# Optimization experiments

Measured on AMD Instinct MI355X. Metric: run time of the kernel, lower is better.

## Reference

```python
import jax, jax.numpy as jnp
import numpy as np

N_BRANCH, N_LAYER = 4, 3
B, T, D_IN = 4, 1024, 32
D_MODEL, D_INNER, D_STATE, D_CONV, DT_RANK = 128, 256, 16, 4, 8
EMBED = 64
MAX_NORM = 10.0  # safe_expmap0 tangent-norm clip
EPS = 1e-7


def setup_inputs() -> dict:
    key = jax.random.key(0)
    ks = jax.random.split(key, 12)
    def nrm(k, shp, s=0.02):
        return s * jax.random.normal(k, shp, dtype=jnp.float32)
    A_init = jnp.log(jnp.arange(1, D_STATE + 1, dtype=jnp.float32))
    return {
        "trend": jax.random.normal(ks[0], (B, T, D_IN), jnp.float32),
        "seasonal_coarse": jax.random.normal(ks[1], (B, T, D_IN), jnp.float32),
        "seasonal_fine": jax.random.normal(ks[2], (B, T, D_IN), jnp.float32),
        "residual": jax.random.normal(ks[3], (B, T, D_IN), jnp.float32),
        "W_ip": nrm(ks[4], (N_BRANCH, D_IN, D_MODEL)),
        "b_ip": jnp.zeros((N_BRANCH, D_MODEL), jnp.float32),
        "W_in": nrm(ks[5], (N_BRANCH, N_LAYER, D_MODEL, 2 * D_INNER)),
        "conv_w": nrm(ks[6], (N_BRANCH, N_LAYER, D_INNER, D_CONV), 0.1),
        "conv_b": jnp.zeros((N_BRANCH, N_LAYER, D_INNER), jnp.float32),
        "W_x": nrm(ks[7], (N_BRANCH, N_LAYER, D_INNER, DT_RANK + 2 * D_STATE)),
        "W_dt": nrm(ks[8], (N_BRANCH, N_LAYER, DT_RANK, D_INNER), 0.1),
        "b_dt": jnp.full((N_BRANCH, N_LAYER, D_INNER), -4.6, jnp.float32),  # softplus ~ 0.01
        "A_log": jnp.broadcast_to(A_init, (N_BRANCH, N_LAYER, D_INNER, D_STATE)),
        "D_param": jnp.ones((N_BRANCH, N_LAYER, D_INNER), jnp.float32),
        "W_out": nrm(ks[9], (N_BRANCH, N_LAYER, D_INNER, D_MODEL)),
        "W_op": nrm(ks[10], (N_BRANCH, D_MODEL, EMBED)),
        "b_op": jnp.zeros((N_BRANCH, EMBED), jnp.float32),
        "eff_scale": jnp.asarray(0.1, jnp.float32),
    }


def _mamba_layer(x, Win, cw, cb, Wx, Wdt, bdt, Alog, Dp, Wout):
    # x: [B, T, d_model]
    Tlen = x.shape[1]
    xz = x @ Win                                   # [B,T,2*di]
    xp, z = jnp.split(xz, 2, axis=-1)
    # causal depthwise conv1d, kernel D_CONV
    xpad = jnp.pad(xp, ((0, 0), (D_CONV - 1, 0), (0, 0)))
    xc = sum(xpad[:, k:k + Tlen, :] * cw[:, k] for k in range(D_CONV))
    xc = jax.nn.silu(xc + cb)                      # [B,T,di]
    dbl = xc @ Wx                                  # [B,T,r+2s]
    dt = jax.nn.softplus(dbl[..., :DT_RANK] @ Wdt + bdt)   # [B,T,di]
    Bm = dbl[..., DT_RANK:DT_RANK + D_STATE]       # [B,T,s]
    Cm = dbl[..., DT_RANK + D_STATE:]              # [B,T,s]
    A = -jnp.exp(Alog)                             # [di,s]
    dA = jnp.exp(dt[..., None] * A)                # [B,T,di,s]
    dBx = (dt * xc)[..., None] * Bm[:, :, None, :] # [B,T,di,s]

    def step(h, inp):
        dA_t, dBx_t, C_t = inp
        h = dA_t * h + dBx_t
        return h, jnp.einsum('bds,bs->bd', h, C_t)

    h0 = jnp.zeros((x.shape[0], D_INNER, D_STATE), x.dtype)
    _, ys = jax.lax.scan(step, h0, (jnp.swapaxes(dA, 0, 1),
                                     jnp.swapaxes(dBx, 0, 1),
                                     jnp.swapaxes(Cm, 0, 1)))
    y = jnp.swapaxes(ys, 0, 1) + Dp * xc
    return (y * jax.nn.silu(z)) @ Wout


def _embed(x, Wip, bip, Wins, cws, cbs, Wxs, Wdts, bdts, Alogs, Dps, Wouts, Wop, bop):
    h = x @ Wip + bip
    for l in range(N_LAYER):
        h = _mamba_layer(h, Wins[l], cws[l], cbs[l], Wxs[l], Wdts[l], bdts[l],
                         Alogs[l], Dps[l], Wouts[l])
    return h.mean(axis=1) @ Wop + bop              # [B, EMBED]


def _expmap0(v):
    # safe expmap0 on Lorentz (k=1): clip tangent norm at MAX_NORM
    n = jnp.linalg.norm(v, axis=-1, keepdims=True)
    nc = jnp.clip(n, EPS, MAX_NORM)
    v = v * (nc / jnp.maximum(n, EPS))
    return jnp.concatenate([jnp.cosh(nc), jnp.sinh(nc) / nc * v], axis=-1)


def _projx(x):
    sp = x[..., 1:]
    t = jnp.sqrt(1.0 + jnp.sum(sp * sp, axis=-1, keepdims=True))
    return jnp.concatenate([t, sp], axis=-1)


def _logmap0(x):
    sp = x[..., 1:]
    t = jnp.maximum(x[..., :1], 1.0 + EPS)
    d = jnp.arccosh(t)
    spn = jnp.maximum(jnp.linalg.norm(sp, axis=-1, keepdims=True), EPS)
    return d * sp / spn


def _forward(trend, seasonal_coarse, seasonal_fine, residual,
             W_ip, b_ip, W_in, conv_w, conv_b, W_x, W_dt, b_dt,
             A_log, D_param, W_out, W_op, b_op, eff_scale):
    xs = [trend, seasonal_coarse, seasonal_fine, residual]
    z_t = [
        _embed(xs[b], W_ip[b], b_ip[b], W_in[b], conv_w[b], conv_b[b], W_x[b],
               W_dt[b], b_dt[b], A_log[b], D_param[b], W_out[b], W_op[b], b_op[b])
        for b in range(N_BRANCH)
    ]
    es = jnp.tanh(eff_scale)
    z_h = [_projx(_expmap0(z * es)) for z in z_t]
    us = [_logmap0(zh) for zh in z_h]
    combined_tangent = us[0] + us[1] + us[2] + us[3]
    combined_h = _projx(_expmap0(combined_tangent * es))
    return (*z_t, *z_h, combined_tangent, combined_h)


def reference(trend, seasonal_coarse, seasonal_fine, residual,
              W_ip, b_ip, W_in, conv_w, conv_b, W_x, W_dt, b_dt,
              A_log, D_param, W_out, W_op, b_op, eff_scale):
    return _forward(trend, seasonal_coarse, seasonal_fine, residual,
                    W_ip, b_ip, W_in, conv_w, conv_b, W_x, W_dt, b_dt,
                    A_log, D_param, W_out, W_op, b_op, eff_scale)
```

## Files before the change

kernel.cpp:

```cpp
#include <hip/hip_runtime.h>
#include <math.h>

#define NBR 4
#define NLAY 3
#define Bk 4
#define Tk 1024
#define DIN 32
#define DMODEL 128
#define DINNER 256
#define DSTATE 16
#define DTRANK 8
#define EMBEDk 64
#define BT (Bk*Tk)
#define EPSF 1e-7f
#define MAXNF 10.0f
#define LCH 64
#define NCH (Tk/LCH)
#define UF 8
#define NWB 320

typedef __bf16 bf16x8 __attribute__((ext_vector_type(8)));
typedef float  f32x4  __attribute__((ext_vector_type(4)));
typedef unsigned short u16x8 __attribute__((ext_vector_type(8)));
typedef unsigned short u16x4 __attribute__((ext_vector_type(4)));

__device__ __forceinline__ float siluf(float x){ return x / (1.f + __expf(-x)); }
__device__ __forceinline__ float softplusf(float x){ return (x > 20.f) ? x : log1pf(__expf(x)); }
__device__ __forceinline__ unsigned short f2b(float x){
    union { float f; unsigned u; } v; v.f = x;
    unsigned r = v.u + 0x7FFF + ((v.u >> 16) & 1);
    return (unsigned short)(r >> 16);
}
__device__ __forceinline__ float b2f(unsigned short u){
    union { unsigned u; float f; } v; v.u = ((unsigned)u) << 16; return v.f;
}

__device__ __forceinline__ void gll16(const void* g, void* l){
    __builtin_amdgcn_global_load_lds(
        (const __attribute__((address_space(1))) unsigned int*)g,
        (__attribute__((address_space(3))) unsigned int*)l,
        16, 0, 0);
}

__device__ __forceinline__ void dA_pow(float q, float* dA){
    dA[0] = q;             dA[1] = q * q;
    dA[2] = dA[1] * dA[0]; dA[3] = dA[1] * dA[1];
    dA[4] = dA[3] * dA[0]; dA[5] = dA[3] * dA[1];
    dA[6] = dA[3] * dA[2]; dA[7] = dA[3] * dA[3];
    #pragma unroll
    for (int s = 8; s < 16; ++s) dA[s] = dA[s - 8] * dA[7];
}
__device__ __forceinline__ void dA_exp(float dtv, const float* Aa, float* dA){
    #pragma unroll
    for (int s = 0; s < 16; ++s) dA[s] = __expf(dtv * Aa[s]);
}

template<int MODE>
__global__ __launch_bounds__(256) void bgemm_k(
    const unsigned short* __restrict__ Ab, long aBr, int K,
    const unsigned short* __restrict__ Bt, long bBr,
    float* __restrict__ C0, long c0Br,
    float* __restrict__ C1, long c1Br,
    unsigned short* __restrict__ Cb, long cbBr,
    const float* __restrict__ bias, long biasBr)
{
    const int br = blockIdx.z;
    Ab += (long)br * aBr;
    Bt += (long)br * bBr;
    if (MODE == 3) C0 += (long)br * c0Br;
    if (MODE == 0 || MODE == 3) C1 += (long)br * c1Br;
    if (MODE == 0) Cb += (long)br * cbBr;
    if (MODE == 3) bias += (long)br * biasBr;
    const int m0 = blockIdx.x * 64, n0 = blockIdx.y * 64;
    __shared__ __align__(16) unsigned short As[8 * 64 * 8];
    __shared__ __align__(16) unsigned short Bs[8 * 64 * 8];
    const int tid = threadIdx.x;
    const int lane = tid & 63, w = tid >> 6;
    const int wm = w >> 1, wn = w & 1;
    const int quad = lane >> 4, l15 = lane & 15;
    f32x4 acc00 = {0,0,0,0}, acc01 = {0,0,0,0}, acc10 = {0,0,0,0}, acc11 = {0,0,0,0};
    for (int kc = 0; kc < K; kc += 64) {
        #pragma unroll
        for (int it = 0; it < 2; ++it) {
            const int kch = w + it * 4;
            gll16(Ab + (long)(m0 + lane) * K + kc + kch * 8, &As[(kch * 64) * 8]);
            gll16(Bt + (long)(n0 + lane) * K + kc + kch * 8, &Bs[(kch * 64) * 8]);
        }
        __syncthreads();
        #pragma unroll
        for (int k0 = 0; k0 < 64; k0 += 32) {
            const int kch = (k0 >> 3) + quad;
            bf16x8 a0 = *(const bf16x8*)&As[(kch * 64 + wm * 32 +      l15) * 8];
            bf16x8 a1 = *(const bf16x8*)&As[(kch * 64 + wm * 32 + 16 + l15) * 8];
            bf16x8 b0 = *(const bf16x8*)&Bs[(kch * 64 + wn * 32 +      l15) * 8];
            bf16x8 b1 = *(const bf16x8*)&Bs[(kch * 64 + wn * 32 + 16 + l15) * 8];
            acc00 = __builtin_amdgcn_mfma_f32_16x16x32_bf16(a0, b0, acc00, 0, 0, 0);
            acc01 = __builtin_amdgcn_mfma_f32_16x16x32_bf16(a0, b1, acc01, 0, 0, 0);
            acc10 = __builtin_amdgcn_mfma_f32_16x16x32_bf16(a1, b0, acc10, 0, 0, 0);
            acc11 = __builtin_amdgcn_mfma_f32_16x16x32_bf16(a1, b1, acc11, 0, 0, 0);
        }
        __syncthreads();
    }
    #pragma unroll
    for (int e = 0; e < 4; ++e) {
        f32x4 a = (e == 0) ? acc00 : (e == 1) ? acc01 : (e == 2) ? acc10 : acc11;
        const int msub = (e >> 1) * 16, nsub = (e & 1) * 16;
        const int col = n0 + wn * 32 + nsub + l15;
        #pragma unroll
        for (int r = 0; r < 4; ++r) {
            const int row = m0 + wm * 32 + msub + quad * 4 + r;
            const float v = a[r];
            if (MODE == 0) {
                if (n0 < 256) Cb[(long)row * 256 + col] = f2b(v);
                else          C1[(long)row * 256 + (col - 256)] = siluf(v);
            } else {
                if (col < 256)      C0[(long)row * 256 + col] = softplusf(v + bias[col]);
                else if (col < 288) C1[(long)row * 32 + (col - 256)] = v;
            }
        }
    }
}

__global__ __launch_bounds__(256) void sgemmWT_k(
    const float* __restrict__ Wout, const float* __restrict__ Win,
    const float* __restrict__ Wip, const float* __restrict__ bip,
    const float* __restrict__ Wop,
    unsigned short* __restrict__ WfT, float* __restrict__ Weq,
    float* __restrict__ Wcomb)
{
    const int z = blockIdx.z;
    const int tid = threadIdx.x;
    const int tx = tid & 15, ty = tid >> 4;
    __shared__ float As_[32][68];
    __shared__ float Bs_[32][68];
    float acc[4][4] = {};
    if (z < 8) {
        const int p = z >> 2, br = z & 3;
        const float* A  = Wout + (long)(br * NLAY + p) * DINNER * DMODEL;
        const float* Bw = Win  + (long)(br * NLAY + p + 1) * DMODEL * 512;
        const int m0 = blockIdx.x * 64, n0 = blockIdx.y * 64;
        for (int kc = 0; kc < DMODEL; kc += 32) {
            #pragma unroll
            for (int it = 0; it < 2; ++it) {
                int id = tid + it * 256;
                int r = id >> 3, c4 = (id & 7) << 2;
                float4 v = *(const float4*)(A + (long)(m0 + r) * DMODEL + kc + c4);
                As_[c4+0][r] = v.x; As_[c4+1][r] = v.y; As_[c4+2][r] = v.z; As_[c4+3][r] = v.w;
                int rb = id >> 4, cb = (id & 15) << 2;
                *(float4*)&Bs_[rb][cb] = *(const float4*)(Bw + (long)(kc + rb) * 512 + n0 + cb);
            }
            __syncthreads();
            #pragma unroll
            for (int kk = 0; kk < 32; ++kk) {
                float4 a4 = *(const float4*)&As_[kk][ty << 2];
                float4 b4 = *(const float4*)&Bs_[kk][tx << 2];
                float av[4] = {a4.x, a4.y, a4.z, a4.w};
                float bv[4] = {b4.x, b4.y, b4.z, b4.w};
                #pragma unroll
                for (int i = 0; i < 4; ++i)
                    #pragma unroll
                    for (int j = 0; j < 4; ++j)
                        acc[i][j] = fmaf(av[i], bv[j], acc[i][j]);
            }
            __syncthreads();
        }
        unsigned short* o = WfT + (long)z * 512 * 256;
        const int row0 = m0 + (ty << 2), col = n0 + (tx << 2);
        #pragma unroll
        for (int j = 0; j < 4; ++j) {
            u16x4 v;
            #pragma unroll
            for (int i = 0; i < 4; ++i) v[i] = f2b(acc[i][j]);
            *(u16x4*)(o + (long)(col + j) * 256 + row0) = v;
        }
    } else if (z == 8) {
        const int br = blockIdx.x;
        const float* A  = Wip + (long)br * DIN * DMODEL;
        const float* bp = bip + (long)br * DMODEL;
        const float* Bw = Win + (long)br * NLAY * DMODEL * 512;
        const int n0 = blockIdx.y * 64;
        for (int kc = 0; kc < DMODEL; kc += 32) {
            #pragma unroll
            for (int it = 0; it < 2; ++it) {
                int id = tid + it * 256;
                int r = id >> 3, c4 = (id & 7) << 2;
                float4 v;
                if (r < 32)       v = *(const float4*)(A + (long)r * DMODEL + kc + c4);
                else if (r == 32) v = *(const float4*)(bp + kc + c4);
                else              { v.x = 0.f; v.y = 0.f; v.z = 0.f; v.w = 0.f; }
                As_[c4+0][r] = v.x; As_[c4+1][r] = v.y; As_[c4+2][r] = v.z; As_[c4+3][r] = v.w;
                int rb = id >> 4, cb = (id & 15) << 2;
                *(float4*)&Bs_[rb][cb] = *(const float4*)(Bw + (long)(kc + rb) * 512 + n0 + cb);
            }
            __syncthreads();
            #pragma unroll
            for (int kk = 0; kk < 32; ++kk) {
                float4 a4 = *(const float4*)&As_[kk][ty << 2];
                float4 b4 = *(const float4*)&Bs_[kk][tx << 2];
                float av[4] = {a4.x, a4.y, a4.z, a4.w};
                float bv[4] = {b4.x, b4.y, b4.z, b4.w};
                #pragma unroll
                for (int i = 0; i < 4; ++i)
                    #pragma unroll
                    for (int j = 0; j < 4; ++j)
                        acc[i][j] = fmaf(av[i], bv[j], acc[i][j]);
            }
            __syncthreads();
        }
        float* C = Weq + (long)br * 33 * 512;
        const int col = n0 + (tx << 2);
        #pragma unroll
        for (int i = 0; i < 4; ++i) {
            const int row = (ty << 2) + i;
            if (row < 33) {
                float4 v4; v4.x = acc[i][0]; v4.y = acc[i][1]; v4.z = acc[i][2]; v4.w = acc[i][3];
                *(float4*)(C + (long)row * 512 + col) = v4;
            }
        }
    } else {
        if (blockIdx.y >= 4) return;
        const int br = blockIdx.y;
        const float* A  = Wout + (long)(br * NLAY + 2) * DINNER * DMODEL;
        const float* Bw = Wop  + (long)br * DMODEL * EMBEDk;
        const int m0 = blockIdx.x * 64;
        for (int kc = 0; kc < DMODEL; kc += 32) {
            #pragma unroll
            for (int it = 0; it < 2; ++it) {
                int id = tid + it * 256;
                int r = id >> 3, c4 = (id & 7) << 2;
                float4 v = *(const float4*)(A + (long)(m0 + r) * DMODEL + kc + c4);
                As_[c4+0][r] = v.x; As_[c4+1][r] = v.y; As_[c4+2][r] = v.z; As_[c4+3][r] = v.w;
                int rb = id >> 4, cb = (id & 15) << 2;
                if (cb < 64)
                    *(float4*)&Bs_[rb][cb] = *(const float4*)(Bw + (long)(kc + rb) * EMBEDk + cb);
            }
            __syncthreads();
            #pragma unroll
            for (int kk = 0; kk < 32; ++kk) {
                float4 a4 = *(const float4*)&As_[kk][ty << 2];
                float4 b4 = *(const float4*)&Bs_[kk][tx << 2];
                float av[4] = {a4.x, a4.y, a4.z, a4.w};
                float bv[4] = {b4.x, b4.y, b4.z, b4.w};
                #pragma unroll
                for (int i = 0; i < 4; ++i)
                    #pragma unroll
                    for (int j = 0; j < 4; ++j)
                        acc[i][j] = fmaf(av[i], bv[j], acc[i][j]);
            }
            __syncthreads();
        }
        float* C = Wcomb + (long)br * DINNER * EMBEDk;
        const int col = tx << 2;
        #pragma unroll
        for (int i = 0; i < 4; ++i) {
            const int row = m0 + (ty << 2) + i;
            float4 v4; v4.x = acc[i][0]; v4.y = acc[i][1]; v4.z = acc[i][2]; v4.w = acc[i][3];
            *(float4*)(C + (long)row * EMBEDk + col) = v4;
        }
    }
}

__global__ __launch_bounds__(256) void prepC_k(
    const float* __restrict__ Wx, const float* __restrict__ Wdt,
    unsigned short* __restrict__ o)
{
    const int n = blockIdx.x, bl = blockIdx.y;
    const int k = threadIdx.x;
    const float* WxP = Wx + (long)bl * DINNER * 40;
    float v;
    if (n < 256) {
        const float* WdtP = Wdt + (long)bl * DTRANK * DINNER;
        float s = 0.f;
        #pragma unroll
        for (int r = 0; r < 8; ++r) s = fmaf(WxP[k * 40 + r], WdtP[r * DINNER + n], s);
        v = s;
    } else if (n < 288) {
        v = WxP[k * 40 + 8 + (n - 256)];
    } else {
        v = 0.f;
    }
    o[(long)bl * NWB * DINNER + (long)n * DINNER + k] = f2b(v);
}

__global__ __launch_bounds__(256) void xgemm0_k(
    const float* __restrict__ A0, const float* __restrict__ A1,
    const float* __restrict__ A2, const float* __restrict__ A3,
    const float* __restrict__ Weq,
    float* __restrict__ zb, unsigned short* __restrict__ xpb)
{
    const int br = blockIdx.z;
    const float* A = (br == 1) ? A1 : (br == 2) ? A2 : (br == 3) ? A3 : A0;
    const float* W = Weq + (long)br * 33 * 512;
    float* C1 = zb + (long)br * BT * DINNER;
    unsigned short* Cb = xpb + (long)br * BT * DINNER;
    const int m0 = blockIdx.x * 64, n0 = blockIdx.y * 64;
    __shared__ float As_[32][68];
    __shared__ float Bs_[32][68];
    const int tid = threadIdx.x;
    const int tx = tid & 15, ty = tid >> 4;
    float acc[4][4] = {};
    {
        #pragma unroll
        for (int it = 0; it < 2; ++it) {
            int id = tid + it * 256;
            int r = id >> 3, c4 = (id & 7) << 2;
            float4 v = *(const float4*)(A + (long)(m0 + r) * DIN + c4);
            As_[c4+0][r] = v.x; As_[c4+1][r] = v.y; As_[c4+2][r] = v.z; As_[c4+3][r] = v.w;
            int rb = id >> 4, cb = (id & 15) << 2;
            *(float4*)&Bs_[rb][cb] = *(const float4*)(W + (long)rb * 512 + n0 + cb);
        }
        __syncthreads();
        #pragma unroll
        for (int kk = 0; kk < 32; ++kk) {
            float4 a4 = *(const float4*)&As_[kk][ty << 2];
            float4 b4 = *(const float4*)&Bs_[kk][tx << 2];
            float av[4] = {a4.x, a4.y, a4.z, a4.w};
            float bv[4] = {b4.x, b4.y, b4.z, b4.w};
            #pragma unroll
            for (int i = 0; i < 4; ++i)
                #pragma unroll
                for (int j = 0; j < 4; ++j)
                    acc[i][j] = fmaf(av[i], bv[j], acc[i][j]);
        }
    }
    const int col = n0 + (tx << 2);
    float be[4];
    #pragma unroll
    for (int j = 0; j < 4; ++j) be[j] = W[32 * 512 + col + j];
    #pragma unroll
    for (int i = 0; i < 4; ++i) {
        const int row = m0 + (ty << 2) + i;
        #pragma unroll
        for (int j = 0; j < 4; ++j) {
            const float v = acc[i][j] + be[j];
            if (n0 < 256) Cb[(long)row * 256 + col + j] = f2b(v);
            else          C1[(long)row * 256 + (col - 256 + j)] = siluf(v);
        }
    }
}

__global__ __launch_bounds__(256) void conv_k(
    const unsigned short* __restrict__ xp, const float* __restrict__ cw,
    const float* __restrict__ cb, unsigned short* __restrict__ xcb, int layer)
{
    const int br = blockIdx.y;
    const long base = (long)br * BT * DINNER;
    const long idx8 = ((long)blockIdx.x * 256 + threadIdx.x) * 8;
    const int d0 = (int)(idx8 & (DINNER - 1));
    const long row = idx8 >> 8;
    const int t = (int)(row & (Tk - 1));
    const float* cwp = cw + ((long)(br * NLAY + layer) * DINNER + d0) * 4;
    const float* cbp = cb + (long)(br * NLAY + layer) * DINNER + d0;
    u16x8 in[4];
    #pragma unroll
    for (int k = 0; k < 4; ++k) {
        const int tt = t + k - 3;
        if (tt >= 0) {
            in[k] = *(const u16x8*)(xp + base + idx8 + (long)(k - 3) * DINNER);
        } else {
            #pragma unroll
            for (int j = 0; j < 8; ++j) in[k][j] = 0;
        }
    }
    u16x8 o;
    #pragma unroll
    for (int j = 0; j < 8; ++j) {
        float acc = cbp[j];
        #pragma unroll
        for (int k = 0; k < 4; ++k)
            acc = fmaf(b2f(in[k][j]), cwp[j * 4 + k], acc);
        o[j] = f2b(siluf(acc));
    }
    *(u16x8*)(xcb + base + idx8) = o;
}

__global__ __launch_bounds__(256) void scan1_k(
    const float* __restrict__ dtb, const unsigned short* __restrict__ xcb,
    const float* __restrict__ bcb, const float* __restrict__ Alog,
    float* __restrict__ recbuf, int layer)
{
    const int c = blockIdx.x, b = blockIdx.y, br = blockIdx.z;
    const int d = threadIdx.x;
    const float* Ap = Alog + ((long)(br * NLAY + layer) * DINNER + d) * DSTATE;
    float Aa[16];
    bool pw = true;
    #pragma unroll
    for (int s = 0; s < 16; ++s) {
        Aa[s] = -__expf(Ap[s]);
        pw = pw && (fabsf(Aa[s] + (float)(s + 1)) < 1e-3f);
    }
    const long rbase = (long)br * BT + (long)b * Tk + (long)c * LCH;
    const float* dtp = dtb + rbase * DINNER + d;
    const unsigned short* xcp = xcb + rbase * DINNER + d;
    __shared__ float bcs[LCH * 32];
    {
        const float4* g = (const float4*)(bcb + rbase * 32);
        float4* l = (float4*)bcs;
        l[d] = g[d]; l[d + 256] = g[d + 256];
    }
    float dtc[UF], xcc[UF];
    #pragma unroll
    for (int u = 0; u < UF; ++u) {
        dtc[u] = dtp[(long)u * DINNER];
        xcc[u] = b2f(xcp[(long)u * DINNER]);
    }
    __syncthreads();
    float h[16];
    #pragma unroll
    for (int s = 0; s < 16; ++s) h[s] = 0.f;
    float sumdt = 0.f;
    for (int base = 0; base < LCH; base += UF) {
        const int nb = (base + UF < LCH) ? base + UF : base;
        float dtn[UF], xcn[UF];
        #pragma unroll
        for (int u = 0; u < UF; ++u) {
            dtn[u] = dtp[(long)(nb + u) * DINNER];
            xcn[u] = b2f(xcp[(long)(nb + u) * DINNER]);
        }
        #pragma unroll
        for (int u = 0; u < UF; ++u) {
            const int t = base + u;
            const float dtv = dtc[u];
            const float dtxc = dtv * xcc[u];
            sumdt += dtv;
            float dA[16];
            if (pw) dA_pow(__expf(-dtv), dA);
            else    dA_exp(dtv, Aa, dA);
            const float* bcT = bcs + t * 32;
            #pragma unroll
            for (int s = 0; s < 16; ++s)
                h[s] = fmaf(dA[s], h[s], dtxc * bcT[s]);
        }
        #pragma unroll
        for (int u = 0; u < UF; ++u) { dtc[u] = dtn[u]; xcc[u] = xcn[u]; }
    }
    float* sb = recbuf + (((long)(br * 4 + b) * (NCH - 1) + c) * 17) * 256 + d;
    #pragma unroll
    for (int s = 0; s < 16; ++s) sb[s * 256] = h[s];
    sb[16 * 256] = sumdt;
}

__global__ __launch_bounds__(256) void scan3_k(
    const float* __restrict__ dtb, const unsigned short* __restrict__ xcb,
    const float* __restrict__ bcb, const float* __restrict__ zb,
    const float* __restrict__ Alog, const float* __restrict__ Dpar,
    const float* __restrict__ recbuf, unsigned short* __restrict__ yzb, int layer)
{
    const int c = blockIdx.x, b = blockIdx.y, br = blockIdx.z;
    const int d = threadIdx.x;
    const float* Ap = Alog + ((long)(br * NLAY + layer) * DINNER + d) * DSTATE;
    float Aa[16];
    bool pw = true;
    #pragma unroll
    for (int s = 0; s < 16; ++s) {
        Aa[s] = -__expf(Ap[s]);
        pw = pw && (fabsf(Aa[s] + (float)(s + 1)) < 1e-3f);
    }
    float h[16];
    #pragma unroll
    for (int s = 0; s < 16; ++s) h[s] = 0.f;
    if (c > 0) {
        const float* recB = recbuf + ((long)(br * 4 + b) * (NCH - 1)) * 17 * 256 + d;
        float rh[16], rs;
        #pragma unroll
        for (int s = 0; s < 16; ++s) rh[s] = recB[s * 256];
        rs = recB[16 * 256];
        for (int cc = 0; cc < c; ++cc) {
            float nh[16], ns = 0.f;
            if (cc + 1 < c) {
                const float* r2 = recB + (long)(cc + 1) * 17 * 256;
                #pragma unroll
                for (int s = 0; s < 16; ++s) nh[s] = r2[s * 256];
                ns = r2[16 * 256];
            } else {
                #pragma unroll
                for (int s = 0; s < 16; ++s) nh[s] = 0.f;
            }
            float P[16];
            if (pw) dA_pow(__expf(-rs), P);
            else    dA_exp(rs, Aa, P);
            #pragma unroll
            for (int s = 0; s < 16; ++s) h[s] = fmaf(h[s], P[s], rh[s]);
            #pragma unroll
            for (int s = 0; s < 16; ++s) rh[s] = nh[s];
            rs = ns;
        }
    }
    const float Dp = Dpar[(br * NLAY + layer) * DINNER + d];
    const long rbase = (long)br * BT + (long)b * Tk + (long)c * LCH;
    const float* dtp = dtb + rbase * DINNER + d;
    const unsigned short* xcp = xcb + rbase * DINNER + d;
    const float* zp  = zb  + rbase * DINNER + d;
    unsigned short* yp = yzb + rbase * DINNER + d;
    __shared__ float bcs[LCH * 32];
    {
        const float4* g = (const float4*)(bcb + rbase * 32);
        float4* l = (float4*)bcs;
        l[d] = g[d]; l[d + 256] = g[d + 256];
    }
    float dtc[UF], xcc[UF], zc[UF];
    #pragma unroll
    for (int u = 0; u < UF; ++u) {
        dtc[u] = dtp[(long)u * DINNER];
        xcc[u] = b2f(xcp[(long)u * DINNER]);
        zc[u]  = zp[(long)u * DINNER];
    }
    __syncthreads();
    for (int base = 0; base < LCH; base += UF) {
        const int nb = (base + UF < LCH) ? base + UF : base;
        float dtn[UF], xcn[UF], zn[UF];
        #pragma unroll
        for (int u = 0; u < UF; ++u) {
            dtn[u] = dtp[(long)(nb + u) * DINNER];
            xcn[u] = b2f(xcp[(long)(nb + u) * DINNER]);
            zn[u]  = zp[(long)(nb + u) * DINNER];
        }
        #pragma unroll
        for (int u = 0; u < UF; ++u) {
            const int t = base + u;
            const float dtv = dtc[u], xcv = xcc[u];
            const float dtxc = dtv * xcv;
            float dA[16];
            if (pw) dA_pow(__expf(-dtv), dA);
            else    dA_exp(dtv, Aa, dA);
            const float* bcT = bcs + t * 32;
            #pragma unroll
            for (int s = 0; s < 16; ++s)
                h[s] = fmaf(dA[s], h[s], dtxc * bcT[s]);
            float y0 = 0.f, y1 = 0.f, y2 = 0.f, y3 = 0.f;
            #pragma unroll
            for (int s = 0; s < 16; s += 4) {
                y0 = fmaf(h[s+0], bcT[16+s+0], y0);
                y1 = fmaf(h[s+1], bcT[16+s+1], y1);
                y2 = fmaf(h[s+2], bcT[16+s+2], y2);
                y3 = fmaf(h[s+3], bcT[16+s+3], y3);
            }
            const float y = (y0 + y1) + (y2 + y3) + Dp * xcv;
            yp[(long)t * DINNER] = f2b(y * zc[u]);
        }
        #pragma unroll
        for (int u = 0; u < UF; ++u) { dtc[u] = dtn[u]; xcc[u] = xcn[u]; zc[u] = zn[u]; }
    }
}

__global__ __launch_bounds__(256) void csum1_k(
    const unsigned short* __restrict__ yz, float* __restrict__ part)
{
    const int ch = blockIdx.x, brb = blockIdx.y;
    const int br = brb >> 2, b = brb & 3;
    const long rbase = (long)br * BT + (long)b * Tk + (long)ch * 128;
    const int tid = threadIdx.x;
    const int cg = tid & 31;
    const int ro = tid >> 5;
    const unsigned short* p = yz + (rbase + ro) * DINNER + cg * 8;
    float acc[8] = {0,0,0,0,0,0,0,0};
    for (int it = 0; it < 16; ++it) {
        u16x8 v = *(const u16x8*)(p + (long)it * 8 * DINNER);
        #pragma unroll
        for (int j = 0; j < 8; ++j) acc[j] += b2f(v[j]);
    }
    __shared__ float sm[8][256];
    #pragma unroll
    for (int j = 0; j < 8; ++j) sm[ro][cg * 8 + j] = acc[j];
    __syncthreads();
    float s = 0.f;
    #pragma unroll
    for (int r = 0; r < 8; ++r) s += sm[r][tid];
    part[((long)brb * 8 + ch) * 256 + tid] = s;
}

__global__ __launch_bounds__(256) void csum2_k(
    const float* __restrict__ part, const float* __restrict__ Wcomb,
    const float* __restrict__ bop, float* __restrict__ outzt)
{
    const int brb = blockIdx.x, br = brb >> 2;
    const int tid = threadIdx.x;
    __shared__ float vm[256];
    __shared__ float red[4][64];
    float s = 0.f;
    #pragma unroll
    for (int ch = 0; ch < 8; ++ch) s += part[((long)brb * 8 + ch) * 256 + tid];
    vm[tid] = s * (1.0f / Tk);
    __syncthreads();
    const float* Wc = Wcomb + (long)br * DINNER * EMBEDk;
    const int col = tid & 63, seg = tid >> 6;
    float a = 0.f;
    #pragma unroll 8
    for (int k = seg * 64; k < seg * 64 + 64; ++k)
        a = fmaf(vm[k], Wc[(long)k * EMBEDk + col], a);
    red[seg][col] = a;
    __syncthreads();
    if (tid < 64)
        outzt[brb * EMBEDk + tid] =
            red[0][tid] + red[1][tid] + red[2][tid] + red[3][tid] + bop[br * EMBEDk + tid];
}

__global__ __launch_bounds__(64) void final_k(
    const float* __restrict__ zt, float* __restrict__ out, const float* __restrict__ eff)
{
    const float es = tanhf(eff[0]);
    __shared__ float us[NBR][Bk][EMBEDk];
    const int t = threadIdx.x;
    if (t < 16) {
        const int br = t >> 2, b = t & 3;
        const float* z = zt + br * (Bk * EMBEDk) + b * EMBEDk;
        float n2 = 0.f;
        for (int e = 0; e < EMBEDk; ++e) { float v = z[e] * es; n2 = fmaf(v, v, n2); }
        const float n  = sqrtf(n2);
        const float nc = fminf(fmaxf(n, EPSF), MAXNF);
        const float sc = nc / fmaxf(n, EPSF);
        const float sh = sinhf(nc) / nc;
        const float fac = es * sc * sh;
        float* zh = out + 1024 + br * (Bk * (EMBEDk + 1)) + b * (EMBEDk + 1);
        float sp2 = 0.f;
        for (int e = 0; e < EMBEDk; ++e) {
            float spv = z[e] * fac;
            sp2 = fmaf(spv, spv, sp2);
            zh[1 + e] = spv;
            us[br][b][e] = spv;
        }
        const float t0 = sqrtf(1.f + sp2);
        zh[0] = t0;
        const float dd  = acoshf(fmaxf(t0, 1.f + EPSF));
        const float spn = fmaxf(sqrtf(sp2), EPSF);
        const float rr  = dd / spn;
        for (int e = 0; e < EMBEDk; ++e) us[br][b][e] *= rr;
    }
    __syncthreads();
    if (t < 4) {
        const int b = t;
        float ct[EMBEDk];
        float* cto = out + 2064 + b * EMBEDk;
        for (int e = 0; e < EMBEDk; ++e) {
            float v = us[0][b][e] + us[1][b][e] + us[2][b][e] + us[3][b][e];
            ct[e] = v; cto[e] = v;
        }
        float n2 = 0.f;
        for (int e = 0; e < EMBEDk; ++e) { float v = ct[e] * es; n2 = fmaf(v, v, n2); }
        const float n  = sqrtf(n2);
        const float nc = fminf(fmaxf(n, EPSF), MAXNF);
        const float sc = nc / fmaxf(n, EPSF);
        const float sh = sinhf(nc) / nc;
        const float fac = es * sc * sh;
        float* ch = out + 2320 + b * (EMBEDk + 1);
        float sp2 = 0.f;
        for (int e = 0; e < EMBEDk; ++e) {
            float spv = ct[e] * fac;
            sp2 = fmaf(spv, spv, sp2);
            ch[1 + e] = spv;
        }
        ch[0] = sqrtf(1.f + sp2);
    }
}

extern "C" void kernel_launch(void* const* d_in, const int* in_sizes, int n_in,
                              void* d_out, int out_size, void* d_ws, size_t ws_size,
                              hipStream_t stream)
{
    const float* X0 = (const float*)d_in[0];
    const float* X1 = (const float*)d_in[1];
    const float* X2 = (const float*)d_in[2];
    const float* X3 = (const float*)d_in[3];
    const float* W_ip   = (const float*)d_in[4];
    const float* b_ip   = (const float*)d_in[5];
    const float* W_in   = (const float*)d_in[6];
    const float* conv_w = (const float*)d_in[7];
    const float* conv_b = (const float*)d_in[8];
    const float* W_x    = (const float*)d_in[9];
    const float* W_dt   = (const float*)d_in[10];
    const float* b_dt   = (const float*)d_in[11];
    const float* A_log  = (const float*)d_in[12];
    const float* D_par  = (const float*)d_in[13];
    const float* W_out  = (const float*)d_in[14];
    const float* W_op   = (const float*)d_in[15];
    const float* b_op   = (const float*)d_in[16];
    const float* eff    = (const float*)d_in[17];
    float* out = (float*)d_out;
    float* ws  = (float*)d_ws;

    float* buf_z  = ws;
    float* buf_dt = buf_z  + (long)NBR * BT * DINNER;
    float* buf_bc = buf_dt + (long)NBR * BT * DINNER;
    float* part   = buf_bc + (long)NBR * BT * 32;
    float* recbuf = part   + 32768;
    float* Weq    = recbuf + (long)16 * (NCH - 1) * 17 * 256;
    float* Wcomb  = Weq + 4 * 33 * 512;
    unsigned short* xp_bf = (unsigned short*)(Wcomb + 4 * 256 * 64);
    unsigned short* xc_bf = xp_bf + (long)NBR * BT * DINNER;
    unsigned short* yz_bf = xc_bf + (long)NBR * BT * DINNER;
    unsigned short* WfT   = yz_bf + (long)NBR * BT * DINNER;
    unsigned short* WcT   = WfT   + (long)8 * 512 * DINNER;

    prepC_k<<<dim3(NWB, NBR * NLAY), 256, 0, stream>>>(W_x, W_dt, WcT);
    sgemmWT_k<<<dim3(4, 8, 10), 256, 0, stream>>>(
        W_out, W_in, W_ip, b_ip, W_op, WfT, Weq, Wcomb);

    xgemm0_k<<<dim3(BT / 64, 8, NBR), 256, 0, stream>>>(
        X0, X1, X2, X3, Weq, buf_z, xp_bf);

    for (int l = 0; l < NLAY; ++l) {
        if (l > 0) {
            bgemm_k<0><<<dim3(BT / 64, 8, NBR), 256, 0, stream>>>(
                yz_bf, (long)BT * DINNER, DINNER,
                WfT + (long)(l - 1) * 4 * 512 * DINNER, (long)512 * DINNER,
                nullptr, 0, buf_z, (long)BT * DINNER,
                xp_bf, (long)BT * DINNER, nullptr, 0);
        }
        conv_k<<<dim3((BT * DINNER) / (256 * 8), NBR), 256, 0, stream>>>(
            xp_bf, conv_w, conv_b, xc_bf, l);
        bgemm_k<3><<<dim3(BT / 64, NWB / 64, NBR), 256, 0, stream>>>(
            xc_bf, (long)BT * DINNER, DINNER,
            WcT + (long)l * NWB * DINNER, (long)NLAY * NWB * DINNER,
            buf_dt, (long)BT * DINNER, buf_bc, (long)BT * 32,
            nullptr, 0, b_dt + l * DINNER, (long)NLAY * DINNER);
        scan1_k<<<dim3(NCH - 1, Bk, NBR), 256, 0, stream>>>(
            buf_dt, xc_bf, buf_bc, A_log, recbuf, l);
        scan3_k<<<dim3(NCH, Bk, NBR), 256, 0, stream>>>(
            buf_dt, xc_bf, buf_bc, buf_z, A_log, D_par, recbuf, yz_bf, l);
    }

    csum1_k<<<dim3(8, 16), 256, 0, stream>>>(yz_bf, part);
    csum2_k<<<16, 256, 0, stream>>>(part, Wcomb, b_op, out);
    final_k<<<1, 64, 0, stream>>>(out, out, eff);
}
```

Measured before the change: 429.9 us.

## Fuse two-pass chunked scan into one kernel with flag-based cross-block handoff

Merges scan1_k and scan3_k into a single scan_k. Each block computes its chunk-local state, publishes it to recbuf, and raises a release flag. Later blocks spin on acquire loads of those flags before combining prefix states and doing the output pass. The dt and z intermediates are now stored in bf16 instead of fp32, and the block's dt, xc and bc tiles are staged once in shared memory with async loads so both passes reuse them. This cuts one launch and roughly halves intermediate traffic, but it relies on co-residency to avoid deadlock in the spin-wait and adds bf16 rounding to dt and z.

```diff
diff --git a/kernel.cpp b/kernel.cpp
--- a/kernel.cpp
+++ b/kernel.cpp
@@ -59,18 +59,17 @@
 __global__ __launch_bounds__(256) void bgemm_k(
     const unsigned short* __restrict__ Ab, long aBr, int K,
     const unsigned short* __restrict__ Bt, long bBr,
-    float* __restrict__ C0, long c0Br,
-    float* __restrict__ C1, long c1Br,
-    unsigned short* __restrict__ Cb, long cbBr,
+    unsigned short* __restrict__ Cu0, long cu0Br,
+    unsigned short* __restrict__ Cu1, long cu1Br,
+    float* __restrict__ Cf, long cfBr,
     const float* __restrict__ bias, long biasBr)
 {
     const int br = blockIdx.z;
     Ab += (long)br * aBr;
     Bt += (long)br * bBr;
-    if (MODE == 3) C0 += (long)br * c0Br;
-    if (MODE == 0 || MODE == 3) C1 += (long)br * c1Br;
-    if (MODE == 0) Cb += (long)br * cbBr;
-    if (MODE == 3) bias += (long)br * biasBr;
+    Cu0 += (long)br * cu0Br;
+    if (MODE == 0) Cu1 += (long)br * cu1Br;
+    if (MODE == 3) { Cf += (long)br * cfBr; bias += (long)br * biasBr; }
     const int m0 = blockIdx.x * 64, n0 = blockIdx.y * 64;
     __shared__ __align__(16) unsigned short As[8 * 64 * 8];
     __shared__ __align__(16) unsigned short Bs[8 * 64 * 8];
@@ -111,11 +110,11 @@
             const int row = m0 + wm * 32 + msub + quad * 4 + r;
             const float v = a[r];
             if (MODE == 0) {
-                if (n0 < 256) Cb[(long)row * 256 + col] = f2b(v);
-                else          C1[(long)row * 256 + (col - 256)] = siluf(v);
+                if (n0 < 256) Cu0[(long)row * 256 + col] = f2b(v);
+                else          Cu1[(long)row * 256 + (col - 256)] = f2b(siluf(v));
             } else {
-                if (col < 256)      C0[(long)row * 256 + col] = softplusf(v + bias[col]);
-                else if (col < 288) C1[(long)row * 32 + (col - 256)] = v;
+                if (col < 256)      Cu0[(long)row * 256 + col] = f2b(softplusf(v + bias[col]));
+                else if (col < 288) Cf[(long)row * 32 + (col - 256)] = v;
             }
         }
     }
@@ -286,12 +285,12 @@
     const float* __restrict__ A0, const float* __restrict__ A1,
     const float* __restrict__ A2, const float* __restrict__ A3,
     const float* __restrict__ Weq,
-    float* __restrict__ zb, unsigned short* __restrict__ xpb)
+    unsigned short* __restrict__ zb, unsigned short* __restrict__ xpb)
 {
     const int br = blockIdx.z;
     const float* A = (br == 1) ? A1 : (br == 2) ? A2 : (br == 3) ? A3 : A0;
     const float* W = Weq + (long)br * 33 * 512;
-    float* C1 = zb + (long)br * BT * DINNER;
+    unsigned short* Cz = zb + (long)br * BT * DINNER;
     unsigned short* Cb = xpb + (long)br * BT * DINNER;
     const int m0 = blockIdx.x * 64, n0 = blockIdx.y * 64;
     __shared__ float As_[32][68];
@@ -334,7 +333,7 @@
         for (int j = 0; j < 4; ++j) {
             const float v = acc[i][j] + be[j];
             if (n0 < 256) Cb[(long)row * 256 + col + j] = f2b(v);
-            else          C1[(long)row * 256 + (col - 256 + j)] = siluf(v);
+            else          Cz[(long)row * 256 + (col - 256 + j)] = f2b(siluf(v));
         }
     }
 }
@@ -374,93 +373,88 @@
     *(u16x8*)(xcb + base + idx8) = o;
 }
 
-__global__ __launch_bounds__(256) void scan1_k(
-    const float* __restrict__ dtb, const unsigned short* __restrict__ xcb,
-    const float* __restrict__ bcb, const float* __restrict__ Alog,
-    float* __restrict__ recbuf, int layer)
+__global__ __launch_bounds__(256) void scan_k(
+    const unsigned short* __restrict__ dtb, const unsigned short* __restrict__ xcb,
+    const float* __restrict__ bcb, const unsigned short* __restrict__ zb,
+    const float* __restrict__ Alog, const float* __restrict__ Dpar,
+    float* __restrict__ recbuf, int* __restrict__ flags,
+    unsigned short* __restrict__ yzb, int layer)
 {
     const int c = blockIdx.x, b = blockIdx.y, br = blockIdx.z;
-    const int d = threadIdx.x;
-    const float* Ap = Alog + ((long)(br * NLAY + layer) * DINNER + d) * DSTATE;
-    float Aa[16];
-    bool pw = true;
+    const int tid = threadIdx.x, d = tid;
+    const int lane = tid & 63, w = tid >> 6;
+    const int bl = br * NLAY + layer;
+    __shared__ __align__(16) unsigned short dts[LCH * DINNER];
+    __shared__ __align__(16) unsigned short xcs[LCH * DINNER];
+    __shared__ __align__(16) float bcs[LCH * 32];
+    const long rbase = (long)br * BT + (long)b * Tk + (long)c * LCH;
+    {
+        const unsigned short* dtG = dtb + rbase * DINNER;
+        const unsigned short* xcG = xcb + rbase * DINNER;
+        const float* bcG = bcb + rbase * 32;
+        #pragma unroll
+        for (int it = 0; it < 8; ++it) {
+            const int unitW = it * 256 + w * 64;
+            gll16(dtG + (long)(unitW + lane) * 8, &dts[unitW * 8]);
+            gll16(xcG + (long)(unitW + lane) * 8, &xcs[unitW * 8]);
+        }
+        #pragma unroll
+        for (int it = 0; it < 2; ++it) {
+            const int unitW = it * 256 + w * 64;
+            gll16(bcG + (long)(unitW + lane) * 4, &bcs[unitW * 4]);
+        }
+    }
+    const float* Ap = Alog + ((long)bl * DINNER + d) * DSTATE;
+    float Aa[16]; bool pw = true;
     #pragma unroll
     for (int s = 0; s < 16; ++s) {
         Aa[s] = -__expf(Ap[s]);
         pw = pw && (fabsf(Aa[s] + (float)(s + 1)) < 1e-3f);
     }
-    const long rbase = (long)br * BT + (long)b * Tk + (long)c * LCH;
-    const float* dtp = dtb + rbase * DINNER + d;
-    const unsigned short* xcp = xcb + rbase * DINNER + d;
-    __shared__ float bcs[LCH * 32];
-    {
-        const float4* g = (const float4*)(bcb + rbase * 32);
-        float4* l = (float4*)bcs;
-        l[d] = g[d]; l[d + 256] = g[d + 256];
-    }
-    float dtc[UF], xcc[UF];
-    #pragma unroll
-    for (int u = 0; u < UF; ++u) {
-        dtc[u] = dtp[(long)u * DINNER];
-        xcc[u] = b2f(xcp[(long)u * DINNER]);
-    }
     __syncthreads();
-    float h[16];
-    #pragma unroll
-    for (int s = 0; s < 16; ++s) h[s] = 0.f;
-    float sumdt = 0.f;
-    for (int base = 0; base < LCH; base += UF) {
-        const int nb = (base + UF < LCH) ? base + UF : base;
-        float dtn[UF], xcn[UF];
-        #pragma unroll
-        for (int u = 0; u < UF; ++u) {
-            dtn[u] = dtp[(long)(nb + u) * DINNER];
-            xcn[u] = b2f(xcp[(long)(nb + u) * DINNER]);
-        }
-        #pragma unroll
-        for (int u = 0; u < UF; ++u) {
-            const int t = base + u;
-            const float dtv = dtc[u];
-            const float dtxc = dtv * xcc[u];
+
+    const int gidx = (br * 4 + b) * 16;
+    const long recstride = 17 * 256;
+
+    if (c < NCH - 1) {
+        float h[16];
+        #pragma unroll
+        for (int s = 0; s < 16; ++s) h[s] = 0.f;
+        float sumdt = 0.f;
+        #pragma unroll 4
+        for (int t = 0; t < LCH; ++t) {
+            const float dtv = b2f(dts[t * 256 + d]);
+            const float xcv = b2f(xcs[t * 256 + d]);
+            const float dtxc = dtv * xcv;
             sumdt += dtv;
             float dA[16];
-            if (pw) dA_pow(__expf(-dtv), dA);
-            else    dA_exp(dtv, Aa, dA);
+            if (pw) dA_pow(__expf(-dtv), dA); else dA_exp(dtv, Aa, dA);
             const float* bcT = bcs + t * 32;
             #pragma unroll
-            for (int s = 0; s < 16; ++s)
-                h[s] = fmaf(dA[s], h[s], dtxc * bcT[s]);
-        }
-        #pragma unroll
-        for (int u = 0; u < UF; ++u) { dtc[u] = dtn[u]; xcc[u] = xcn[u]; }
-    }
-    float* sb = recbuf + (((long)(br * 4 + b) * (NCH - 1) + c) * 17) * 256 + d;
-    #pragma unroll
-    for (int s = 0; s < 16; ++s) sb[s * 256] = h[s];
-    sb[16 * 256] = sumdt;
-}
-
-__global__ __launch_bounds__(256) void scan3_k(
-    const float* __restrict__ dtb, const unsigned short* __restrict__ xcb,
-    const float* __restrict__ bcb, const float* __restrict__ zb,
-    const float* __restrict__ Alog, const float* __restrict__ Dpar,
-    const float* __restrict__ recbuf, unsigned short* __restrict__ yzb, int layer)
-{
-    const int c = blockIdx.x, b = blockIdx.y, br = blockIdx.z;
-    const int d = threadIdx.x;
-    const float* Ap = Alog + ((long)(br * NLAY + layer) * DINNER + d) * DSTATE;
-    float Aa[16];
-    bool pw = true;
-    #pragma unroll
-    for (int s = 0; s < 16; ++s) {
-        Aa[s] = -__expf(Ap[s]);
-        pw = pw && (fabsf(Aa[s] + (float)(s + 1)) < 1e-3f);
-    }
-    float h[16];
-    #pragma unroll
-    for (int s = 0; s < 16; ++s) h[s] = 0.f;
+            for (int s = 0; s < 16; ++s) h[s] = fmaf(dA[s], h[s], dtxc * bcT[s]);
+        }
+        float* sb = recbuf + ((long)(br * 4 + b) * (NCH - 1) + c) * recstride + d;
+        #pragma unroll
+        for (int s = 0; s < 16; ++s) sb[s * 256] = h[s];
+        sb[16 * 256] = sumdt;
+        __threadfence();
+        __syncthreads();
+        if (tid == 0)
+            __hip_atomic_store(&flags[gidx + c], 1, __ATOMIC_RELEASE, __HIP_MEMORY_SCOPE_AGENT);
+    }
+
+    float hc[16];
+    #pragma unroll
+    for (int s = 0; s < 16; ++s) hc[s] = 0.f;
     if (c > 0) {
-        const float* recB = recbuf + ((long)(br * 4 + b) * (NCH - 1)) * 17 * 256 + d;
+        if (tid == 0) {
+            for (int cc = 0; cc < c; ++cc)
+                while (__hip_atomic_load(&flags[gidx + cc], __ATOMIC_ACQUIRE, __HIP_MEMORY_SCOPE_AGENT) == 0)
+                    __builtin_amdgcn_s_sleep(2);
+        }
+        __syncthreads();
+        __threadfence();
+        const float* recB = recbuf + (long)(br * 4 + b) * (NCH - 1) * recstride + d;
         float rh[16], rs;
         #pragma unroll
         for (int s = 0; s < 16; ++s) rh[s] = recB[s * 256];
@@ -468,7 +462,7 @@
         for (int cc = 0; cc < c; ++cc) {
             float nh[16], ns = 0.f;
             if (cc + 1 < c) {
-                const float* r2 = recB + (long)(cc + 1) * 17 * 256;
+                const float* r2 = recB + (long)(cc + 1) * recstride;
                 #pragma unroll
                 for (int s = 0; s < 16; ++s) nh[s] = r2[s * 256];
                 ns = r2[16 * 256];
@@ -477,69 +471,55 @@
                 for (int s = 0; s < 16; ++s) nh[s] = 0.f;
             }
             float P[16];
-            if (pw) dA_pow(__expf(-rs), P);
-            else    dA_exp(rs, Aa, P);
-            #pragma unroll
-            for (int s = 0; s < 16; ++s) h[s] = fmaf(h[s], P[s], rh[s]);
+            if (pw) dA_pow(__expf(-rs), P); else dA_exp(rs, Aa, P);
+            #pragma unroll
+            for (int s = 0; s < 16; ++s) hc[s] = fmaf(hc[s], P[s], rh[s]);
             #pragma unroll
             for (int s = 0; s < 16; ++s) rh[s] = nh[s];
             rs = ns;
         }
     }
-    const float Dp = Dpar[(br * NLAY + layer) * DINNER + d];
-    const long rbase = (long)br * BT + (long)b * Tk + (long)c * LCH;
-    const float* dtp = dtb + rbase * DINNER + d;
-    const unsigned short* xcp = xcb + rbase * DINNER + d;
-    const float* zp  = zb  + rbase * DINNER + d;
-    unsigned short* yp = yzb + rbase * DINNER + d;
-    __shared__ float bcs[LCH * 32];
+
     {
-        const float4* g = (const float4*)(bcb + rbase * 32);
-        float4* l = (float4*)bcs;
-        l[d] = g[d]; l[d + 256] = g[d + 256];
-    }
-    float dtc[UF], xcc[UF], zc[UF];
-    #pragma unroll
-    for (int u = 0; u < UF; ++u) {
-        dtc[u] = dtp[(long)u * DINNER];
-        xcc[u] = b2f(xcp[(long)u * DINNER]);
-        zc[u]  = zp[(long)u * DINNER];
-    }
-    __syncthreads();
-    for (int base = 0; base < LCH; base += UF) {
-        const int nb = (base + UF < LCH) ? base + UF : base;
-        float dtn[UF], xcn[UF], zn[UF];
-        #pragma unroll
-        for (int u = 0; u < UF; ++u) {
-            dtn[u] = dtp[(long)(nb + u) * DINNER];
-            xcn[u] = b2f(xcp[(long)(nb + u) * DINNER]);
-            zn[u]  = zp[(long)(nb + u) * DINNER];
-        }
-        #pragma unroll
-        for (int u = 0; u < UF; ++u) {
-            const int t = base + u;
-            const float dtv = dtc[u], xcv = xcc[u];
-            const float dtxc = dtv * xcv;
-            float dA[16];
-            if (pw) dA_pow(__expf(-dtv), dA);
-            else    dA_exp(dtv, Aa, dA);
-            const float* bcT = bcs + t * 32;
-            #pragma unroll
-            for (int s = 0; s < 16; ++s)
-                h[s] = fmaf(dA[s], h[s], dtxc * bcT[s]);
-            float y0 = 0.f, y1 = 0.f, y2 = 0.f, y3 = 0.f;
-            #pragma unroll
-            for (int s = 0; s < 16; s += 4) {
-                y0 = fmaf(h[s+0], bcT[16+s+0], y0);
-                y1 = fmaf(h[s+1], bcT[16+s+1], y1);
-                y2 = fmaf(h[s+2], bcT[16+s+2], y2);
-                y3 = fmaf(h[s+3], bcT[16+s+3], y3);
-            }
-            const float y = (y0 + y1) + (y2 + y3) + Dp * xcv;
-            yp[(long)t * DINNER] = f2b(y * zc[u]);
-        }
-        #pragma unroll
-        for (int u = 0; u < UF; ++u) { dtc[u] = dtn[u]; xcc[u] = xcn[u]; zc[u] = zn[u]; }
+        const float Dp = Dpar[bl * DINNER + d];
+        const unsigned short* zp = zb + rbase * DINNER + d;
+        unsigned short* yp = yzb + rbase * DINNER + d;
+        float h[16];
+        #pragma unroll
+        for (int s = 0; s < 16; ++s) h[s] = hc[s];
+        float zc[UF];
+        #pragma unroll
+        for (int u = 0; u < UF; ++u) zc[u] = b2f(zp[(long)u * DINNER]);
+        for (int base = 0; base < LCH; base += UF) {
+            const int nb = (base + UF < LCH) ? base + UF : base;
+            float zn[UF];
+            #pragma unroll
+            for (int u = 0; u < UF; ++u) zn[u] = b2f(zp[(long)(nb + u) * DINNER]);
+            #pragma unroll
+            for (int u = 0; u < UF; ++u) {
+                const int t = base + u;
+                const float dtv = b2f(dts[t * 256 + d]);
+                const float xcv = b2f(xcs[t * 256 + d]);
+                const float dtxc = dtv * xcv;
+                float dA[16];
+                if (pw) dA_pow(__expf(-dtv), dA); else dA_exp(dtv, Aa, dA);
+                const float* bcT = bcs + t * 32;
+                #pragma unroll
+                for (int s = 0; s < 16; ++s) h[s] = fmaf(dA[s], h[s], dtxc * bcT[s]);
+                float y0 = 0.f, y1 = 0.f, y2 = 0.f, y3 = 0.f;
+                #pragma unroll
+                for (int s = 0; s < 16; s += 4) {
+                    y0 = fmaf(h[s+0], bcT[16+s+0], y0);
+                    y1 = fmaf(h[s+1], bcT[16+s+1], y1);
+                    y2 = fmaf(h[s+2], bcT[16+s+2], y2);
+                    y3 = fmaf(h[s+3], bcT[16+s+3], y3);
+                }
+                const float y = (y0 + y1) + (y2 + y3) + Dp * xcv;
+                yp[(long)t * DINNER] = f2b(y * zc[u]);
+            }
+            #pragma unroll
+            for (int u = 0; u < UF; ++u) zc[u] = zn[u];
+        }
     }
 }
 
@@ -678,45 +658,50 @@
     float* out = (float*)d_out;
     float* ws  = (float*)d_ws;
 
-    float* buf_z  = ws;
-    float* buf_dt = buf_z  + (long)NBR * BT * DINNER;
-    float* buf_bc = buf_dt + (long)NBR * BT * DINNER;
+    float* buf_bc = ws;
     float* part   = buf_bc + (long)NBR * BT * 32;
-    float* recbuf = part   + 32768;
+    float* recbuf = part + 32768;
     float* Weq    = recbuf + (long)16 * (NCH - 1) * 17 * 256;
     float* Wcomb  = Weq + 4 * 33 * 512;
-    unsigned short* xp_bf = (unsigned short*)(Wcomb + 4 * 256 * 64);
+    int*   flags  = (int*)(Wcomb + 4 * 256 * 64);
+    unsigned short* xp_bf = (unsigned short*)(flags + 768);
     unsigned short* xc_bf = xp_bf + (long)NBR * BT * DINNER;
-    unsigned short* yz_bf = xc_bf + (long)NBR * BT * DINNER;
+    unsigned short* z_bf  = xc_bf + (long)NBR * BT * DINNER;
+    unsigned short* dt_bf = z_bf  + (long)NBR * BT * DINNER;
+    unsigned short* yz_bf = dt_bf + (long)NBR * BT * DINNER;
     unsigned short* WfT   = yz_bf + (long)NBR * BT * DINNER;
     unsigned short* WcT   = WfT   + (long)8 * 512 * DINNER;
+
+    hipMemsetAsync(flags, 0, NLAY * 256 * sizeof(int), stream);
 
     prepC_k<<<dim3(NWB, NBR * NLAY), 256, 0, stream>>>(W_x, W_dt, WcT);
     sgemmWT_k<<<dim3(4, 8, 10), 256, 0, stream>>>(
         W_out, W_in, W_ip, b_ip, W_op, WfT, Weq, Wcomb);
 
     xgemm0_k<<<dim3(BT / 64, 8, NBR), 256, 0, stream>>>(
-        X0, X1, X2, X3, Weq, buf_z, xp_bf);
+        X0, X1, X2, X3, Weq, z_bf, xp_bf);
 
     for (int l = 0; l < NLAY; ++l) {
         if (l > 0) {
             bgemm_k<0><<<dim3(BT / 64, 8, NBR), 256, 0, stream>>>(
                 yz_bf, (long)BT * DINNER, DINNER,
                 WfT + (long)(l - 1) * 4 * 512 * DINNER, (long)512 * DINNER,
-                nullptr, 0, buf_z, (long)BT * DINNER,
-                xp_bf, (long)BT * DINNER, nullptr, 0);
+                xp_bf, (long)BT * DINNER,
+                z_bf, (long)BT * DINNER,
+                nullptr, 0, nullptr, 0);
         }
         conv_k<<<dim3((BT * DINNER) / (256 * 8), NBR), 256, 0, stream>>>(
             xp_bf, conv_w, conv_b, xc_bf, l);
         bgemm_k<3><<<dim3(BT / 64, NWB / 64, NBR), 256, 0, stream>>>(
             xc_bf, (long)BT * DINNER, DINNER,
             WcT + (long)l * NWB * DINNER, (long)NLAY * NWB * DINNER,
-            buf_dt, (long)BT * DINNER, buf_bc, (long)BT * 32,
-            nullptr, 0, b_dt + l * DINNER, (long)NLAY * DINNER);
-        scan1_k<<<dim3(NCH - 1, Bk, NBR), 256, 0, stream>>>(
-            buf_dt, xc_bf, buf_bc, A_log, recbuf, l);
-        scan3_k<<<dim3(NCH, Bk, NBR), 256, 0, stream>>>(
-            buf_dt, xc_bf, buf_bc, buf_z, A_log, D_par, recbuf, yz_bf, l);
+            dt_bf, (long)BT * DINNER,
+            nullptr, 0,
+            buf_bc, (long)BT * 32,
+            b_dt + l * DINNER, (long)NLAY * DINNER);
+        scan_k<<<dim3(NCH, Bk, NBR), 256, 0, stream>>>(
+            dt_bf, xc_bf, buf_bc, z_bf, A_log, D_par,
+            recbuf, flags + l * 256, yz_bf, l);
     }
 
     csum1_k<<<dim3(8, 16), 256, 0, stream>>>(yz_bf, part);
```

New measurement: 652.9 us. +51.9%, slower.
